# Kernel optimization log

Measured on AMD Instinct MI355X. Metric: run time of the kernel, lower is better.

## Reference

```python
import jax, jax.numpy as jnp
import numpy as np

B, H, W, D = 64, 32, 32, 64
K = 1024  # codebook_size


def setup_inputs() -> dict:
    key = jax.random.key(0)
    kz, ke = jax.random.split(key)
    z = jax.random.normal(kz, (B, H, W, D), dtype=jnp.float32)
    embeddings = 0.02 * jax.random.normal(ke, (K, D), dtype=jnp.float32)
    return {"z": z, "embeddings": embeddings}


def reference(z, embeddings):
    # Flatten spatial/batch dims: (N, D) with N = B*H*W
    z_flat = z.reshape(-1, z.shape[-1])
    # Squared euclidean distances via ||a||^2 + ||b||^2 - 2 a.b  -> (N, K)
    distances = (jnp.sum(z_flat ** 2, axis=1, keepdims=True)
                 + jnp.sum(embeddings ** 2, axis=1)
                 - 2.0 * jnp.dot(z_flat, embeddings.T))
    indices = jnp.argmin(distances, axis=1)  # (N,)
    quantized = embeddings[indices].reshape(z.shape)  # (B, H, W, D)
    indices = indices.reshape(z.shape[0], z.shape[1], z.shape[2])  # (B, H, W)
    return quantized, indices
```

## Files before the change

kernel.cpp:

```cpp
#include <hip/hip_runtime.h>

#define NPTS   65536
#define DDIM   64
#define KCODES 1024
#define QOUT_ELEMS (NPTS * DDIM)

typedef _Float16 half8    __attribute__((ext_vector_type(8)));
typedef float    floatx16 __attribute__((ext_vector_type(16)));
typedef unsigned int uint;

#define AS1 __attribute__((address_space(1)))
#define AS3 __attribute__((address_space(3)))

#define WS_EHP   0
#define WS_ELP   (128*1024)
#define WS_E2    (256*1024)

static __device__ __forceinline__ void gl_lds16(const void* g, void* l) {
    __builtin_amdgcn_global_load_lds((const AS1 uint*)g, (AS3 uint*)l, 16, 0, 0);
}

__global__ void eprep_kernel(const float* __restrict__ emb, char* __restrict__ ws) {
    const int tid = threadIdx.x;
    const int w = tid >> 6, d = tid & 63;
    const int k = blockIdx.x * 4 + w;
    float v = emb[(size_t)k * DDIM + d];
    _Float16 h = (_Float16)v;
    _Float16 l = (_Float16)(v - (float)h);
    size_t off = (size_t)(k >> 5) * 4096 + (size_t)(d >> 3) * 512
               + (size_t)(k & 31) * 16 + (size_t)(d & 7) * 2;
    *(_Float16*)(ws + WS_EHP + off) = h;
    *(_Float16*)(ws + WS_ELP + off) = l;
    float s = v * v;
    #pragma unroll
    for (int m = 1; m < 64; m <<= 1) s += __shfl_xor(s, m, 64);
    if (d == 0) ((float*)(ws + WS_E2))[k] = s;
}

#define MFMA(A,B,C) __builtin_amdgcn_mfma_f32_32x32x16_f16(A,B,C,0,0,0)

__global__ __launch_bounds__(256, 2) void vq_kernel(
    const float* __restrict__ z,
    const char* __restrict__ ws_c,
    const float* __restrict__ emb,
    float* __restrict__ out)
{
    const int tid  = threadIdx.x;
    const int lane = tid & 63;
    const int w    = __builtin_amdgcn_readfirstlane(tid >> 6);
    const int col  = lane & 31;
    const int sel8 = lane >> 5;
    const int pgrp = blockIdx.x;

    __shared__ char  ebuf[4][8192];
    __shared__ float lds_e2[1024];
    __shared__ int   s_final[128];

    const int pt = pgrp * 128 + w * 32 + col;
    half8 ah[4], al[4];
    {
        const float* zrow = z + (size_t)pt * DDIM + sel8 * 8;
        #pragma unroll
        for (int ks = 0; ks < 4; ++ks) {
            float4 u0 = *(const float4*)(zrow + ks * 16);
            float4 u1 = *(const float4*)(zrow + ks * 16 + 4);
            float tv[8] = {u0.x, u0.y, u0.z, u0.w, u1.x, u1.y, u1.z, u1.w};
            #pragma unroll
            for (int j = 0; j < 8; ++j) {
                float a = -2.0f * tv[j];
                _Float16 hh = (_Float16)a;
                ah[ks][j] = hh;
                al[ks][j] = (_Float16)(a - (float)hh);
            }
        }
    }
    asm volatile("s_waitcnt vmcnt(0)" ::: "memory");
    __builtin_amdgcn_sched_barrier(0);

    const floatx16 zeroC = {};

    float best[16];
    int   bt[16];
    #pragma unroll
    for (int r = 0; r < 16; ++r) { best[r] = 3.4e38f; bt[r] = 0; }

    const int opnd = w >> 1, hsel = w & 1;
    const char* gsrc = ws_c + (opnd ? WS_ELP : WS_EHP) + hsel * 2048 + lane * 16;
    char* lbase = &ebuf[0][0] + opnd * 4096 + hsel * 2048;

#define STAGE(BUF, T) do {                                                    \
    const char* _s = gsrc + (size_t)(T) * 4096;                               \
    char* _d = lbase + (BUF) * 8192;                                          \
    gl_lds16(_s,        _d);                                                  \
    gl_lds16(_s + 1024, _d + 1024);                                           \
} while (0)

    const int myoff = sel8 * 512 + col * 16;

#define READF(BUF, T, BH, BL, E2) do {                                        \
    const char* _b = &ebuf[BUF][0] + myoff;                                   \
    _Pragma("unroll")                                                         \
    for (int ks = 0; ks < 4; ++ks) {                                          \
        BH[ks] = *(const half8*)(_b + ks * 1024);                             \
        BL[ks] = *(const half8*)(_b + 4096 + ks * 1024);                      \
    }                                                                         \
    E2 = lds_e2[(T) * 32 + col];                                              \
} while (0)

#define COMP(T, BH, BL, E2) do {                                              \
    __builtin_amdgcn_s_setprio(1);                                            \
    floatx16 c0 = MFMA(ah[0], BH[0], zeroC);                                  \
    floatx16 c1 = MFMA(ah[0], BL[0], zeroC);                                  \
    c0 = MFMA(ah[1], BH[1], c0);  c1 = MFMA(ah[1], BL[1], c1);                \
    c0 = MFMA(ah[2], BH[2], c0);  c1 = MFMA(ah[2], BL[2], c1);                \
    c0 = MFMA(ah[3], BH[3], c0);  c1 = MFMA(ah[3], BL[3], c1);                \
    c0 = MFMA(al[0], BH[0], c0);  c1 = MFMA(al[2], BH[2], c1);                \
    c0 = MFMA(al[1], BH[1], c0);  c1 = MFMA(al[3], BH[3], c1);                \
    __builtin_amdgcn_s_setprio(0);                                            \
    _Pragma("unroll")                                                         \
    for (int r = 0; r < 16; ++r) {                                            \
        float d = (c0[r] + c1[r]) + (E2);                                     \
        bool c = d < best[r];               \
        best[r] = c ? d   : best[r];                                          \
        bt[r]   = c ? (T) : bt[r];                                            \
    }                                                                         \
} while (0)

#define WAITBAR(N) do {                                                       \
    asm volatile("s_waitcnt vmcnt(" #N ") lgkmcnt(0)" ::: "memory");          \
    __builtin_amdgcn_sched_barrier(0);                                        \
    __builtin_amdgcn_s_barrier();                                             \
    __builtin_amdgcn_sched_barrier(0);                                        \
} while (0)

    half8 bhA[4], blA[4], bhB[4], blB[4];
    float e2A, e2B;

    gl_lds16(ws_c + WS_E2 + w * 1024 + lane * 16, (char*)lds_e2 + w * 1024);
    STAGE(0, 0);
    STAGE(1, 1);
    STAGE(2, 2);
    WAITBAR(4);
    READF(0, 0, bhA, blA, e2A);
    STAGE(3, 3);

    #pragma unroll 1
    for (int t = 0; t < 28; t += 2) {
        WAITBAR(4);
        READF((t + 1) & 3, t + 1, bhB, blB, e2B);
        STAGE((t + 4) & 3, t + 4);
        COMP(t, bhA, blA, e2A);

        WAITBAR(4);
        READF((t + 2) & 3, t + 2, bhA, blA, e2A);
        STAGE((t + 5) & 3, t + 5);
        COMP(t + 1, bhB, blB, e2B);
    }

    WAITBAR(4);
    READF(29 & 3, 29, bhB, blB, e2B);
    COMP(28, bhA, blA, e2A);

    WAITBAR(2);
    READF(30 & 3, 30, bhA, blA, e2A);
    COMP(29, bhB, blB, e2B);

    WAITBAR(0);
    READF(31 & 3, 31, bhB, blB, e2B);
    COMP(30, bhA, blA, e2A);

    COMP(31, bhB, blB, e2B);
#undef STAGE
#undef READF
#undef COMP
#undef WAITBAR

    int code[16];
    #pragma unroll
    for (int r = 0; r < 16; ++r) code[r] = bt[r] * 32 + col;
    #pragma unroll
    for (int m = 1; m < 32; m <<= 1) {
        #pragma unroll
        for (int r = 0; r < 16; ++r) {
            float ov = __shfl_xor(best[r], m, 64);
            int   oc = __shfl_xor(code[r], m, 64);
            bool c = (ov < best[r]) || (ov == best[r] && oc < code[r]);
            best[r] = c ? ov : best[r];
            code[r] = c ? oc : code[r];
        }
    }
    if (col == 0) {
        #pragma unroll
        for (int r = 0; r < 16; ++r) {
            int row = (r & 3) + 8 * (r >> 2) + 4 * sel8;
            s_final[w * 32 + row] = code[r];
        }
    }
    __syncthreads();

    if (tid < 128)
        out[QOUT_ELEMS + (size_t)pgrp * 128 + tid] = (float)s_final[tid];
    float4* outq = (float4*)out;
    const float4* emb4 = (const float4*)emb;
    #pragma unroll
    for (int it = 0; it < 8; ++it) {
        int f  = it * 256 + tid;
        int p  = f >> 4;
        int d4 = f & 15;
        int ks = s_final[p];
        outq[((size_t)pgrp * 128 + p) * (DDIM / 4) + d4] =
            emb4[(size_t)ks * (DDIM / 4) + d4];
    }
}

extern "C" void kernel_launch(void* const* d_in, const int* in_sizes, int n_in,
                              void* d_out, int out_size, void* d_ws, size_t ws_size,
                              hipStream_t stream) {
    const float* z   = (const float*)d_in[0];
    const float* emb = (const float*)d_in[1];
    float* out = (float*)d_out;
    char* ws = (char*)d_ws;

    eprep_kernel<<<KCODES / 4, 256, 0, stream>>>(emb, ws);
    vq_kernel<<<NPTS / 128, 256, 0, stream>>>(z, ws, emb, out);
}
```

Baseline: 99.78 us.

## Software-pipeline MFMA chains with the previous tile's argmin update

Splits the per-tile compute into an MFMA chain and an argmin reduction, then reorders the loop so each tile's MFMA chain is issued before the argmin of the previous tile. The aim is to hide MFMA latency behind the VALU compare/select work instead of stalling on the accumulator results. This keeps two sets of 16-wide accumulators live, raising VGPR pressure, which could hurt occupancy under the two-blocks-per-CU launch bound.

After: 102.6 us. +2.9%, slower.

```diff
diff --git a/kernel.cpp b/kernel.cpp
--- a/kernel.cpp
+++ b/kernel.cpp
@@ -78,7 +78,6 @@
     __builtin_amdgcn_sched_barrier(0);
 
     const floatx16 zeroC = {};
-
     float best[16];
     int   bt[16];
     #pragma unroll
@@ -107,19 +106,22 @@
     E2 = lds_e2[(T) * 32 + col];                                              \
 } while (0)
 
-#define COMP(T, BH, BL, E2) do {                                              \
+#define CHAIN(BH, BL, C0, C1) do {                                            \
     __builtin_amdgcn_s_setprio(1);                                            \
-    floatx16 c0 = MFMA(ah[0], BH[0], zeroC);                                  \
-    floatx16 c1 = MFMA(ah[0], BL[0], zeroC);                                  \
-    c0 = MFMA(ah[1], BH[1], c0);  c1 = MFMA(ah[1], BL[1], c1);                \
-    c0 = MFMA(ah[2], BH[2], c0);  c1 = MFMA(ah[2], BL[2], c1);                \
-    c0 = MFMA(ah[3], BH[3], c0);  c1 = MFMA(ah[3], BL[3], c1);                \
-    c0 = MFMA(al[0], BH[0], c0);  c1 = MFMA(al[2], BH[2], c1);                \
-    c0 = MFMA(al[1], BH[1], c0);  c1 = MFMA(al[3], BH[3], c1);                \
+    C0 = MFMA(ah[0], BH[0], zeroC);                                           \
+    C1 = MFMA(ah[0], BL[0], zeroC);                                           \
+    C0 = MFMA(ah[1], BH[1], C0);  C1 = MFMA(ah[1], BL[1], C1);                \
+    C0 = MFMA(ah[2], BH[2], C0);  C1 = MFMA(ah[2], BL[2], C1);                \
+    C0 = MFMA(ah[3], BH[3], C0);  C1 = MFMA(ah[3], BL[3], C1);                \
+    C0 = MFMA(al[0], BH[0], C0);  C1 = MFMA(al[2], BH[2], C1);                \
+    C0 = MFMA(al[1], BH[1], C0);  C1 = MFMA(al[3], BH[3], C1);                \
     __builtin_amdgcn_s_setprio(0);                                            \
+} while (0)
+
+#define ARGMIN(T, C0, C1, E2) do {                                            \
     _Pragma("unroll")                                                         \
     for (int r = 0; r < 16; ++r) {                                            \
-        float d = (c0[r] + c1[r]) + (E2);                                     \
+        float d = (C0[r] + C1[r]) + (E2);                                     \
         bool c = d < best[r];               \
         best[r] = c ? d   : best[r];                                          \
         bt[r]   = c ? (T) : bt[r];                                            \
@@ -134,7 +136,8 @@
 } while (0)
 
     half8 bhA[4], blA[4], bhB[4], blB[4];
-    float e2A, e2B;
+    float e2A, e2B, e2s;
+    floatx16 c0A, c1A, c0B, c1B;
 
     gl_lds16(ws_c + WS_E2 + w * 1024 + lane * 16, (char*)lds_e2 + w * 1024);
     STAGE(0, 0);
@@ -144,35 +147,62 @@
     READF(0, 0, bhA, blA, e2A);
     STAGE(3, 3);
 
+    WAITBAR(4);
+    READF(1, 1, bhB, blB, e2B);
+    STAGE(0, 4);
+    CHAIN(bhA, blA, c0A, c1A);
+
     #pragma unroll 1
-    for (int t = 0; t < 28; t += 2) {
+    for (int t = 1; t < 27; t += 2) {
         WAITBAR(4);
-        READF((t + 1) & 3, t + 1, bhB, blB, e2B);
+        e2s = e2A;
+        READF((t + 1) & 3, t + 1, bhA, blA, e2A);
         STAGE((t + 4) & 3, t + 4);
-        COMP(t, bhA, blA, e2A);
+        CHAIN(bhB, blB, c0B, c1B);
+        ARGMIN(t - 1, c0A, c1A, e2s);
 
         WAITBAR(4);
-        READF((t + 2) & 3, t + 2, bhA, blA, e2A);
+        e2s = e2B;
+        READF((t + 2) & 3, t + 2, bhB, blB, e2B);
         STAGE((t + 5) & 3, t + 5);
-        COMP(t + 1, bhB, blB, e2B);
-    }
-
-    WAITBAR(4);
+        CHAIN(bhA, blA, c0A, c1A);
+        ARGMIN(t, c0B, c1B, e2s);
+    }
+
+    WAITBAR(4);
+    e2s = e2A;
+    READF(28 & 3, 28, bhA, blA, e2A);
+    STAGE(31 & 3, 31);
+    CHAIN(bhB, blB, c0B, c1B);
+    ARGMIN(26, c0A, c1A, e2s);
+
+    WAITBAR(4);
+    e2s = e2B;
     READF(29 & 3, 29, bhB, blB, e2B);
-    COMP(28, bhA, blA, e2A);
+    CHAIN(bhA, blA, c0A, c1A);
+    ARGMIN(27, c0B, c1B, e2s);
 
     WAITBAR(2);
+    e2s = e2A;
     READF(30 & 3, 30, bhA, blA, e2A);
-    COMP(29, bhB, blB, e2B);
+    CHAIN(bhB, blB, c0B, c1B);
+    ARGMIN(28, c0A, c1A, e2s);
 
     WAITBAR(0);
+    e2s = e2B;
     READF(31 & 3, 31, bhB, blB, e2B);
-    COMP(30, bhA, blA, e2A);
-
-    COMP(31, bhB, blB, e2B);
+    CHAIN(bhA, blA, c0A, c1A);
+    ARGMIN(29, c0B, c1B, e2s);
+
+    e2s = e2A;
+    CHAIN(bhB, blB, c0B, c1B);
+    ARGMIN(30, c0A, c1A, e2s);
+
+    ARGMIN(31, c0B, c1B, e2B);
 #undef STAGE
 #undef READF
-#undef COMP
+#undef CHAIN
+#undef ARGMIN
 #undef WAITBAR
 
     int code[16];
```
